# Performance work log

Measured on AMD Instinct MI355X. Metric: run time of the kernel, lower is better.

The kernel has to match this reference:

```python
import jax, jax.numpy as jnp
import numpy as np

S, B, V, E, H, T = 256, 32, 50000, 300, 256, 32  # seq, batch, vocab, emb, lstm hidden, num_tags


def _lstm_dir(x, w_ih, w_hh, b_ih, b_hh, reverse):
    # x: [S, B, in]; gates in PyTorch order i, f, g, o
    Bm, Hm = x.shape[1], w_hh.shape[1]
    def step(carry, xt):
        h, c = carry
        g = xt @ w_ih.T + b_ih + h @ w_hh.T + b_hh  # [B, 4H]
        i, f, gg, o = jnp.split(g, 4, axis=-1)
        c = jax.nn.sigmoid(f) * c + jax.nn.sigmoid(i) * jnp.tanh(gg)
        h = jax.nn.sigmoid(o) * jnp.tanh(c)
        return (h, c), h
    init = (jnp.zeros((Bm, Hm), x.dtype), jnp.zeros((Bm, Hm), x.dtype))
    _, hs = jax.lax.scan(step, init, x, reverse=reverse)
    return hs  # [S, B, H]


def _crf_loss(em, tags, start, trans, end):
    # em: [S, B, T]; torchcrf log-likelihood, reduction='sum', full mask
    bidx = jnp.arange(em.shape[1])
    # numerator (gold path score)
    emit = jnp.take_along_axis(em, tags[:, :, None], axis=2)[..., 0].sum(0)  # [B]
    tr = trans[tags[:-1], tags[1:]].sum(0)  # [B]
    num = start[tags[0]] + emit + tr + end[tags[-1]]
    # denominator (forward algorithm)
    def step(alpha, e):
        alpha = jax.nn.logsumexp(alpha[:, :, None] + trans[None] + e[:, None, :], axis=1)
        return alpha, None
    alpha0 = start[None] + em[0]  # [B, T]
    alpha, _ = jax.lax.scan(step, alpha0, em[1:])
    logZ = jax.nn.logsumexp(alpha + end[None], axis=-1)  # [B]
    return -(num - logZ).sum()


def _viterbi(em, start, trans, end):
    def step(s, e):
        cand = s[:, :, None] + trans[None]           # [B, T_prev, T_cur]
        return cand.max(1) + e, cand.argmax(1)        # score [B,T], backptr [B,T]
    score0 = start[None] + em[0]
    score, hist = jax.lax.scan(step, score0, em[1:])  # hist: [S-1, B, T]
    last = jnp.argmax(score + end[None], axis=-1)     # [B]
    def back(tag, bp):
        prev = jnp.take_along_axis(bp, tag[:, None], axis=1)[:, 0]
        return prev, prev
    _, path_head = jax.lax.scan(back, last, hist, reverse=True)  # [S-1, B]
    return jnp.concatenate([path_head, last[None]], axis=0).astype(jnp.int32)  # [S, B]


def setup_inputs():
    key = jax.random.key(0)
    ks = jax.random.split(key, 32)
    def n(k, shape, s=0.1):
        return (jax.random.normal(k, shape, jnp.float32) * s)
    inp = {
        'words': jax.random.randint(ks[0], (S, B), 0, V),
        'chars': jax.random.randint(ks[1], (S, B, 16), 0, 100),
        'tags': jax.random.randint(ks[2], (S, B), 0, T),
        'emb_table': n(ks[3], (V, E)),
        'fc_w': n(ks[4], (T, 2 * H), float(np.sqrt(2.0 / (T + 2 * H)))),
        'fc_b': n(ks[5], (T,), float(np.sqrt(1.0 / T))),
        'crf_start': n(ks[6], (T,)),
        'crf_end': n(ks[7], (T,)),
        'crf_trans': n(ks[8], (T, T)),
    }
    i = 9
    for l, din in ((0, E), (1, 2 * H)):
        for d in ('f', 'b'):
            inp[f'w_ih_l{l}{d}'] = n(ks[i], (4 * H, din)); i += 1
            inp[f'w_hh_l{l}{d}'] = n(ks[i], (4 * H, H)); i += 1
            inp[f'b_ih_l{l}{d}'] = n(ks[i], (4 * H,)); i += 1
            inp[f'b_hh_l{l}{d}'] = n(ks[i], (4 * H,)); i += 1
    return inp


def reference(words, chars, tags, emb_table, fc_w, fc_b, crf_start, crf_end, crf_trans,
              w_ih_l0f, w_hh_l0f, b_ih_l0f, b_hh_l0f,
              w_ih_l0b, w_hh_l0b, b_ih_l0b, b_hh_l0b,
              w_ih_l1f, w_hh_l1f, b_ih_l1f, b_hh_l1f,
              w_ih_l1b, w_hh_l1b, b_ih_l1b, b_hh_l1b):
    # chars / char CNN are unused in the original forward()
    x = emb_table[words]                                   # [S, B, E]
    h0 = jnp.concatenate([
        _lstm_dir(x, w_ih_l0f, w_hh_l0f, b_ih_l0f, b_hh_l0f, False),
        _lstm_dir(x, w_ih_l0b, w_hh_l0b, b_ih_l0b, b_hh_l0b, True)], axis=-1)
    h1 = jnp.concatenate([
        _lstm_dir(h0, w_ih_l1f, w_hh_l1f, b_ih_l1f, b_hh_l1f, False),
        _lstm_dir(h0, w_ih_l1b, w_hh_l1b, b_ih_l1b, b_hh_l1b, True)], axis=-1)  # [S, B, 2H]
    em = h1 @ fc_w.T + fc_b                                # emissions [S, B, T]
    crf_out = _viterbi(em, crf_start, crf_trans, crf_end)  # [S, B] int32
    crf_loss = _crf_loss(em, tags, crf_start, crf_trans, crf_end)
    return crf_out, crf_loss
```

## Files before the change

### kernel.cpp

```cpp
#include <hip/hip_runtime.h>
#include <stdint.h>

#define S_ 256
#define B_ 32
#define H_ 256
#define G4_ 1024
#define HXW (16*132)

typedef short bf16x8 __attribute__((ext_vector_type(8)));
typedef float f32x4  __attribute__((ext_vector_type(4)));

__device__ __forceinline__ unsigned f2bf(float f){
  unsigned u = __float_as_uint(f);
  return (u + 0x7fffu + ((u >> 16) & 1u)) >> 16;
}
__device__ __forceinline__ float bfl(unsigned u){ return __uint_as_float(u << 16); }
__device__ __forceinline__ float bfh(unsigned u){ return __uint_as_float(u & 0xffff0000u); }
__device__ __forceinline__ float sigf(float x){ return 1.0f / (1.0f + __expf(-x)); }
__device__ __forceinline__ float thf(float x){
  x = fminf(fmaxf(x, -15.0f), 15.0f);
  float e = __expf(2.0f * x);
  return (e - 1.0f) / (e + 1.0f);
}

__device__ __forceinline__ int hval_ok(unsigned long long v){
  return (((unsigned)v & (unsigned)(v >> 32)) & 0x40004000u) == 0x40004000u;
}

__global__ __launch_bounds__(320) void k_prep(const int* __restrict__ words,
                                              const float* __restrict__ emb,
                                              unsigned short* __restrict__ x,
                                              unsigned* __restrict__ hbuf0){
  int row = blockIdx.x;
  int e = threadIdx.x;
  int w = words[row];
  x[row * 320 + e] = (e < 300) ? (unsigned short)f2bf(emb[w * 300 + e]) : 0;
  if (e < 256) hbuf0[row * 256 + e] = 0;
}

__global__ __launch_bounds__(256) void k_packw(
    const float* __restrict__ w0f, const float* __restrict__ w0b,
    const float* __restrict__ w1f, const float* __restrict__ w1b,
    const float* __restrict__ fw,
    unsigned short* __restrict__ wb0f, unsigned short* __restrict__ wb0b,
    unsigned short* __restrict__ wb1f, unsigned short* __restrict__ wb1b,
    unsigned short* __restrict__ fcwb){
  int r = blockIdx.x, tid = threadIdx.x;
  if (r < 2048){
    int rr = r & 1023;
    const float* src = (r < 1024) ? w0f : w0b;
    unsigned short* dst = (r < 1024) ? wb0f : wb0b;
    for (int e = tid; e < 320; e += 256)
      dst[rr * 320 + e] = (e < 300) ? (unsigned short)f2bf(src[rr * 300 + e]) : 0;
  } else if (r < 4096){
    int rr = r & 1023;
    const float* src = (r < 3072) ? w1f : w1b;
    unsigned short* dst = (r < 3072) ? wb1f : wb1b;
    for (int e = tid; e < 512; e += 256)
      dst[rr * 512 + e] = (unsigned short)f2bf(src[rr * 512 + e]);
  } else {
    int rr = r - 4096;
    for (int e = tid; e < 512; e += 256)
      fcwb[rr * 512 + e] = (unsigned short)f2bf(fw[rr * 512 + e]);
  }
}

__global__ __launch_bounds__(256) void k_gemm_bf2(
    const unsigned short* __restrict__ A, int lda, int nSteps,
    const unsigned short* __restrict__ Bf, const unsigned short* __restrict__ Bb,
    const float* __restrict__ b1f, const float* __restrict__ b2f,
    const float* __restrict__ b1b, const float* __restrict__ b2b,
    float* __restrict__ Cf, float* __restrict__ Cb){
  const int z = blockIdx.z;
  const unsigned short* __restrict__ B = z ? Bb : Bf;
  const float* __restrict__ bias1 = z ? b1b : b1f;
  const float* __restrict__ bias2 = z ? b2b : b2f;
  float* __restrict__ C = z ? Cb : Cf;

  __shared__ __align__(16) unsigned As[64 * 20];
  __shared__ __align__(16) unsigned Bs[128 * 20];
  const int tid = threadIdx.x;
  const int w = tid >> 6, lane = tid & 63;
  const int quad = lane >> 4, coln = lane & 15;
  const int m0 = blockIdx.y * 64, n0 = blockIdx.x * 128;

  f32x4 acc[8];
  #pragma unroll
  for (int i = 0; i < 8; ++i){ acc[i][0]=0.f; acc[i][1]=0.f; acc[i][2]=0.f; acc[i][3]=0.f; }

  for (int kt = 0; kt < nSteps; ++kt){
    int k0 = kt * 32;
    __syncthreads();
    {
      int row = tid >> 2, part = tid & 3;
      *(uint4*)&As[row * 20 + part * 4] =
          *(const uint4*)(A + (size_t)(m0 + row) * lda + k0 + part * 8);
    }
    #pragma unroll
    for (int i = 0; i < 2; ++i){
      int idx = tid + 256 * i;
      int row = idx >> 2, part = idx & 3;
      *(uint4*)&Bs[row * 20 + part * 4] =
          *(const uint4*)(B + (size_t)(n0 + row) * lda + k0 + part * 8);
    }
    __syncthreads();
    union { uint4 q; bf16x8 v; } au;
    au.q = *(const uint4*)&As[(w * 16 + coln) * 20 + quad * 4];
    #pragma unroll
    for (int nt = 0; nt < 8; ++nt){
      union { uint4 q; bf16x8 v; } bu;
      bu.q = *(const uint4*)&Bs[(nt * 16 + coln) * 20 + quad * 4];
      acc[nt] = __builtin_amdgcn_mfma_f32_16x16x32_bf16(au.v, bu.v, acc[nt], 0, 0, 0);
    }
  }
  #pragma unroll
  for (int nt = 0; nt < 8; ++nt){
    int col = n0 + nt * 16 + coln;
    float bs = bias1[col] + bias2[col];
    #pragma unroll
    for (int reg = 0; reg < 4; ++reg)
      C[(size_t)(m0 + w * 16 + quad * 4 + reg) * 1024 + col] = acc[nt][reg] + bs;
  }
}

__global__ __launch_bounds__(256, 1) void k_lstm2(
    const float* __restrict__ Gf, const float* __restrict__ Gb,
    const float* __restrict__ Whf, const float* __restrict__ Whb,
    unsigned* __restrict__ hbuf,
    unsigned short* __restrict__ Hout)
{
  __shared__ __align__(16) unsigned hx[2 * HXW];
  const int wg  = blockIdx.x;
  const int dir = wg >> 3, n = (wg >> 1) & 3, bh = wg & 1;
  const float* __restrict__ G  = dir ? Gb : Gf;
  const float* __restrict__ Wh = dir ? Whb : Whf;
  const int tid  = threadIdx.x;
  const int w    = tid >> 6;
  const int lane = tid & 63;
  const int quad = lane >> 4, coln = lane & 15;

  bf16x8 Wr[32];
  #pragma unroll
  for (int ks = 0; ks < 8; ++ks){
    #pragma unroll
    for (int gt = 0; gt < 4; ++gt){
      const float* wp = Wh + (size_t)(gt * 256 + (n << 6) + (w << 4) + coln) * 256
                        + ks * 32 + quad * 8;
      float4 a = *(const float4*)wp;
      float4 b = *(const float4*)(wp + 4);
      union { unsigned u[4]; bf16x8 v; } tu;
      tu.u[0] = f2bf(a.x) | (f2bf(a.y) << 16);
      tu.u[1] = f2bf(a.z) | (f2bf(a.w) << 16);
      tu.u[2] = f2bf(b.x) | (f2bf(b.y) << 16);
      tu.u[3] = f2bf(b.z) | (f2bf(b.w) << 16);
      Wr[ks * 4 + gt] = tu.v;
    }
  }

  const int gu  = (n << 6) + (w << 4) + coln;
  const int mrw = quad << 2;

  float c0 = 0.f, c1 = 0.f, c2 = 0.f, c3 = 0.f;

  for (int t = 0; t < 256; ++t){
    int s = dir ? (255 - t) : t;
    f32x4 acc[4];
    #pragma unroll
    for (int gt = 0; gt < 4; ++gt){
      const float* gp = G + (size_t)(s * 32 + bh * 16 + mrw) * 1024 + gt * 256 + gu;
      f32x4 a;
      a[0] = gp[0]; a[1] = gp[1024]; a[2] = gp[2048]; a[3] = gp[3072];
      acc[gt] = a;
    }
    unsigned* hxr = &hx[(t & 1) * HXW];
    if (t > 0){
      const unsigned* hb = hbuf + (((size_t)(t - 1) * 2 + dir) * 2 + bh) * 2048;
      int row = tid >> 4, kk = tid & 15;
      int n1 = (n + 1) & 3, n2 = (n + 2) & 3, n3 = (n + 3) & 3;
      const unsigned long long* p1 =
          (const unsigned long long*)(hb + row * 128 + n1 * 32 + kk * 2);
      const unsigned long long* p2 =
          (const unsigned long long*)(hb + row * 128 + n2 * 32 + kk * 2);
      const unsigned long long* p3 =
          (const unsigned long long*)(hb + row * 128 + n3 * 32 + kk * 2);
      unsigned long long v1, v2, v3;
      do {
        v1 = __hip_atomic_load(p1, __ATOMIC_RELAXED, __HIP_MEMORY_SCOPE_AGENT);
        v2 = __hip_atomic_load(p2, __ATOMIC_RELAXED, __HIP_MEMORY_SCOPE_AGENT);
        v3 = __hip_atomic_load(p3, __ATOMIC_RELAXED, __HIP_MEMORY_SCOPE_AGENT);
      } while (!(hval_ok(v1) && hval_ok(v2) && hval_ok(v3)));
      hxr[row * 132 + n1 * 32 + kk * 2]     = (unsigned)v1 & 0xBFFFBFFFu;
      hxr[row * 132 + n1 * 32 + kk * 2 + 1] = (unsigned)(v1 >> 32) & 0xBFFFBFFFu;
      hxr[row * 132 + n2 * 32 + kk * 2]     = (unsigned)v2 & 0xBFFFBFFFu;
      hxr[row * 132 + n2 * 32 + kk * 2 + 1] = (unsigned)(v2 >> 32) & 0xBFFFBFFFu;
      hxr[row * 132 + n3 * 32 + kk * 2]     = (unsigned)v3 & 0xBFFFBFFFu;
      hxr[row * 132 + n3 * 32 + kk * 2 + 1] = (unsigned)(v3 >> 32) & 0xBFFFBFFFu;
      __syncthreads();
      #pragma unroll
      for (int ks = 0; ks < 8; ++ks){
        union { uint4 q; bf16x8 v; } tu;
        tu.q = *(const uint4*)&hxr[coln * 132 + ks * 16 + quad * 4];
        #pragma unroll
        for (int gt = 0; gt < 4; ++gt)
          acc[gt] = __builtin_amdgcn_mfma_f32_16x16x32_bf16(tu.v, Wr[ks * 4 + gt],
                                                            acc[gt], 0, 0, 0);
      }
    }
    unsigned* hxw = &hx[((t + 1) & 1) * HXW];
    unsigned* hw  = hbuf + (((size_t)t * 2 + dir) * 2 + bh) * 2048;
    float cc[4] = {c0, c1, c2, c3};
    #pragma unroll
    for (int reg = 0; reg < 4; ++reg){
      float gi = sigf(acc[0][reg]);
      float gf = sigf(acc[1][reg]);
      float gg = thf (acc[2][reg]);
      float go = sigf(acc[3][reg]);
      float cv = gf * cc[reg] + gi * gg;
      cc[reg] = cv;
      float hv = go * thf(cv);
      unsigned hb16 = f2bf(hv);
      unsigned other = (unsigned)__shfl_xor((int)hb16, 1);
      if (!(coln & 1)){
        unsigned pair = hb16 | (other << 16);
        hxw[(mrw + reg) * 132 + (gu >> 1)] = pair;
        if (t < 255)
          __hip_atomic_store(hw + (mrw + reg) * 128 + (gu >> 1),
                             pair | 0x40004000u,
                             __ATOMIC_RELAXED, __HIP_MEMORY_SCOPE_AGENT);
      }
      Hout[(size_t)(s * 32 + bh * 16 + mrw + reg) * 512 + dir * 256 + gu] =
          (unsigned short)hb16;
    }
    c0 = cc[0]; c1 = cc[1]; c2 = cc[2]; c3 = cc[3];
  }
}

__global__ __launch_bounds__(64) void k_fc(const unsigned short* __restrict__ h1,
                                           const unsigned short* __restrict__ fw,
                                           const float* __restrict__ fb,
                                           float* __restrict__ em){
  int row = blockIdx.x;
  int lane = threadIdx.x;
  int tag = lane & 31, half = lane >> 5;
  const uint4* hp = (const uint4*)(h1 + (size_t)row * 512 + half * 256);
  const uint4* wp = (const uint4*)(fw + (size_t)tag * 512 + half * 256);
  float acc = 0.0f;
  #pragma unroll 8
  for (int i = 0; i < 32; ++i){
    uint4 h = hp[i], v = wp[i];
    acc += bfl(h.x) * bfl(v.x) + bfh(h.x) * bfh(v.x)
         + bfl(h.y) * bfl(v.y) + bfh(h.y) * bfh(v.y)
         + bfl(h.z) * bfl(v.z) + bfh(h.z) * bfh(v.z)
         + bfl(h.w) * bfl(v.w) + bfh(h.w) * bfh(v.w);
  }
  acc += __shfl_down(acc, 32);
  if (half == 0) em[row * 32 + tag] = acc + fb[tag];
}

__global__ __launch_bounds__(64) void k_crf(const float* __restrict__ em,
                                            const int* __restrict__ tags,
                                            const float* __restrict__ start,
                                            const float* __restrict__ trans,
                                            const float* __restrict__ endv,
                                            int* __restrict__ path,
                                            float* __restrict__ lossb){
  __shared__ float tr[1024];
  __shared__ float sc[32], sc2[32];
  __shared__ unsigned char bp[255][32];
  int b = blockIdx.x & 31, mode = blockIdx.x >> 5;
  int t = threadIdx.x;
  for (int i = t; i < 1024; i += 64) tr[i] = trans[i];
  if (t < 32) sc[t] = start[t] + em[b * 32 + t];
  __syncthreads();
  if (mode == 0){
    for (int s = 1; s < 256; ++s){
      if (t < 32){
        float best = -1e30f; int bi = 0;
        for (int p = 0; p < 32; ++p){
          float v = sc[p] + tr[p * 32 + t];
          if (v > best){ best = v; bi = p; }
        }
        sc2[t] = best + em[(s * 32 + b) * 32 + t];
        bp[s - 1][t] = (unsigned char)bi;
      }
      __syncthreads();
      if (t < 32) sc[t] = sc2[t];
      __syncthreads();
    }
    if (t == 0){
      float best = -1e30f; int bi = 0;
      for (int p = 0; p < 32; ++p){
        float v = sc[p] + endv[p];
        if (v > best){ best = v; bi = p; }
      }
      int cur = bi;
      path[255 * 32 + b] = cur;
      for (int s = 254; s >= 0; --s){
        cur = bp[s][cur];
        path[s * 32 + b] = cur;
      }
    }
  } else {
    for (int s = 1; s < 256; ++s){
      if (t < 32){
        float m = -1e30f;
        for (int p = 0; p < 32; ++p){ float v = sc[p] + tr[p * 32 + t]; m = fmaxf(m, v); }
        float ss = 0.0f;
        for (int p = 0; p < 32; ++p){ ss += __expf(sc[p] + tr[p * 32 + t] - m); }
        sc2[t] = m + __logf(ss) + em[(s * 32 + b) * 32 + t];
      }
      __syncthreads();
      if (t < 32) sc[t] = sc2[t];
      __syncthreads();
    }
    float nsum = 0.0f;
    for (int s = t; s < 256; s += 64){
      int tg = tags[s * 32 + b];
      nsum += em[(s * 32 + b) * 32 + tg];
      if (s == 0) nsum += start[tg];
      else        nsum += tr[tags[(s - 1) * 32 + b] * 32 + tg];
      if (s == 255) nsum += endv[tg];
    }
    #pragma unroll
    for (int off = 32; off >= 1; off >>= 1) nsum += __shfl_down(nsum, off);
    if (t == 0){
      float m = -1e30f;
      for (int p = 0; p < 32; ++p) m = fmaxf(m, sc[p] + endv[p]);
      float ss = 0.0f;
      for (int p = 0; p < 32; ++p) ss += __expf(sc[p] + endv[p] - m);
      lossb[b] = m + __logf(ss) - nsum;
    }
  }
}

__global__ __launch_bounds__(64) void k_final(const float* __restrict__ lossb,
                                              float* __restrict__ outp){
  float v = (threadIdx.x < 32) ? lossb[threadIdx.x] : 0.0f;
  #pragma unroll
  for (int off = 32; off >= 1; off >>= 1) v += __shfl_down(v, off);
  if (threadIdx.x == 0) outp[0] = v;
}

extern "C" void kernel_launch(void* const* d_in, const int* in_sizes, int n_in,
                              void* d_out, int out_size, void* d_ws, size_t ws_size,
                              hipStream_t stream){
  const int*   words  = (const int*)d_in[0];
  const int*   tags   = (const int*)d_in[2];
  const float* emb    = (const float*)d_in[3];
  const float* fcw    = (const float*)d_in[4];
  const float* fcb    = (const float*)d_in[5];
  const float* cstart = (const float*)d_in[6];
  const float* cend   = (const float*)d_in[7];
  const float* ctrans = (const float*)d_in[8];
  const float* w_ih[4] = {(const float*)d_in[9],  (const float*)d_in[13],
                          (const float*)d_in[17], (const float*)d_in[21]};
  const float* w_hh[4] = {(const float*)d_in[10], (const float*)d_in[14],
                          (const float*)d_in[18], (const float*)d_in[22]};
  const float* b_ih[4] = {(const float*)d_in[11], (const float*)d_in[15],
                          (const float*)d_in[19], (const float*)d_in[23]};
  const float* b_hh[4] = {(const float*)d_in[12], (const float*)d_in[16],
                          (const float*)d_in[20], (const float*)d_in[24]};

  char* base = (char*)d_ws;
  unsigned short* x    = (unsigned short*)base;
  float* Gf            = (float*)(base + 5242880);
  float* Gb            = (float*)(base + 38797312);
  unsigned short* h0   = (unsigned short*)(base + 72351744);
  unsigned short* h1   = (unsigned short*)(base + 80740352);
  unsigned short* wb0f = (unsigned short*)(base + 89128960);
  unsigned short* wb0b = (unsigned short*)(base + 89784320);
  unsigned short* wb1f = (unsigned short*)(base + 90439680);
  unsigned short* wb1b = (unsigned short*)(base + 91488256);
  unsigned short* fcwb = (unsigned short*)(base + 92536832);
  float* lossb         = (float*)(base + 92569600);
  float* em            = Gf;
  unsigned* hbuf0 = (unsigned*)h1;
  unsigned* hbuf1 = (unsigned*)h0;

  k_prep<<<8192, 320, 0, stream>>>(words, emb, x, hbuf0);
  k_packw<<<4128, 256, 0, stream>>>(w_ih[0], w_ih[1], w_ih[2], w_ih[3], fcw,
                                    wb0f, wb0b, wb1f, wb1b, fcwb);

  k_gemm_bf2<<<dim3(8, 128, 2), 256, 0, stream>>>(x, 320, 10, wb0f, wb0b,
                                                  b_ih[0], b_hh[0], b_ih[1], b_hh[1],
                                                  Gf, Gb);
  k_lstm2<<<16, 256, 0, stream>>>(Gf, Gb, w_hh[0], w_hh[1], hbuf0, h0);

  k_gemm_bf2<<<dim3(8, 128, 2), 256, 0, stream>>>(h0, 512, 16, wb1f, wb1b,
                                                  b_ih[2], b_hh[2], b_ih[3], b_hh[3],
                                                  Gf, Gb);
  k_lstm2<<<16, 256, 0, stream>>>(Gf, Gb, w_hh[2], w_hh[3], hbuf1, h1);

  k_fc<<<8192, 64, 0, stream>>>(h1, fcwb, fcb, em);

  k_crf<<<64, 64, 0, stream>>>(em, tags, cstart, ctrans, cend, (int*)d_out, lossb);
  k_final<<<1, 64, 0, stream>>>(lossb, ((float*)d_out) + (out_size - 1));
}
```

Baseline: 1.498 ms.

## Overlap gate loads with h exchange in LSTM and use MFMA for FC

In the recurrent LSTM kernel, the per-step input-gate loads from G and the previous step's Hout store now happen after the spin-wait on the neighbours' hidden state. This keeps that memory traffic off the critical path before the barrier, and the hbuf atomic stores are issued before the LDS writes. The gate pre-activations are added after the MFMA accumulation rather than used as its initial value. Separately, the FC emission projection is rewritten as a 16x16x32 bf16 MFMA tile kernel with the FC weights staged in LDS, using 128 blocks instead of 8192 tiny ones.

```diff
diff --git a/kernel.cpp b/kernel.cpp
--- a/kernel.cpp
+++ b/kernel.cpp
@@ -161,18 +161,15 @@
   const int mrw = quad << 2;
 
   float c0 = 0.f, c1 = 0.f, c2 = 0.f, c3 = 0.f;
+  unsigned prevH[4];
+  int prevS = -1;
 
   for (int t = 0; t < 256; ++t){
     int s = dir ? (255 - t) : t;
+    unsigned* hxr = &hx[(t & 1) * HXW];
+    float gv[4][4];
     f32x4 acc[4];
-    #pragma unroll
-    for (int gt = 0; gt < 4; ++gt){
-      const float* gp = G + (size_t)(s * 32 + bh * 16 + mrw) * 1024 + gt * 256 + gu;
-      f32x4 a;
-      a[0] = gp[0]; a[1] = gp[1024]; a[2] = gp[2048]; a[3] = gp[3072];
-      acc[gt] = a;
-    }
-    unsigned* hxr = &hx[(t & 1) * HXW];
+
     if (t > 0){
       const unsigned* hb = hbuf + (((size_t)(t - 1) * 2 + dir) * 2 + bh) * 2048;
       int row = tid >> 4, kk = tid & 15;
@@ -189,6 +186,19 @@
         v2 = __hip_atomic_load(p2, __ATOMIC_RELAXED, __HIP_MEMORY_SCOPE_AGENT);
         v3 = __hip_atomic_load(p3, __ATOMIC_RELAXED, __HIP_MEMORY_SCOPE_AGENT);
       } while (!(hval_ok(v1) && hval_ok(v2) && hval_ok(v3)));
+      __builtin_amdgcn_sched_barrier(0);
+
+      #pragma unroll
+      for (int gt = 0; gt < 4; ++gt){
+        const float* gp = G + (size_t)(s * 32 + bh * 16 + mrw) * 1024 + gt * 256 + gu;
+        gv[gt][0] = gp[0]; gv[gt][1] = gp[1024];
+        gv[gt][2] = gp[2048]; gv[gt][3] = gp[3072];
+      }
+      #pragma unroll
+      for (int reg = 0; reg < 4; ++reg)
+        Hout[(size_t)(prevS * 32 + bh * 16 + mrw + reg) * 512 + dir * 256 + gu] =
+            (unsigned short)prevH[reg];
+
       hxr[row * 132 + n1 * 32 + kk * 2]     = (unsigned)v1 & 0xBFFFBFFFu;
       hxr[row * 132 + n1 * 32 + kk * 2 + 1] = (unsigned)(v1 >> 32) & 0xBFFFBFFFu;
       hxr[row * 132 + n2 * 32 + kk * 2]     = (unsigned)v2 & 0xBFFFBFFFu;
@@ -197,6 +207,10 @@
       hxr[row * 132 + n3 * 32 + kk * 2 + 1] = (unsigned)(v3 >> 32) & 0xBFFFBFFFu;
       __syncthreads();
       #pragma unroll
+      for (int gt = 0; gt < 4; ++gt){
+        acc[gt][0] = 0.f; acc[gt][1] = 0.f; acc[gt][2] = 0.f; acc[gt][3] = 0.f;
+      }
+      #pragma unroll
       for (int ks = 0; ks < 8; ++ks){
         union { uint4 q; bf16x8 v; } tu;
         tu.q = *(const uint4*)&hxr[coln * 132 + ks * 16 + quad * 4];
@@ -205,56 +219,98 @@
           acc[gt] = __builtin_amdgcn_mfma_f32_16x16x32_bf16(tu.v, Wr[ks * 4 + gt],
                                                             acc[gt], 0, 0, 0);
       }
-    }
+    } else {
+      #pragma unroll
+      for (int gt = 0; gt < 4; ++gt){
+        const float* gp = G + (size_t)(s * 32 + bh * 16 + mrw) * 1024 + gt * 256 + gu;
+        gv[gt][0] = gp[0]; gv[gt][1] = gp[1024];
+        gv[gt][2] = gp[2048]; gv[gt][3] = gp[3072];
+      }
+      #pragma unroll
+      for (int gt = 0; gt < 4; ++gt){
+        acc[gt][0] = 0.f; acc[gt][1] = 0.f; acc[gt][2] = 0.f; acc[gt][3] = 0.f;
+      }
+    }
+
     unsigned* hxw = &hx[((t + 1) & 1) * HXW];
     unsigned* hw  = hbuf + (((size_t)t * 2 + dir) * 2 + bh) * 2048;
     float cc[4] = {c0, c1, c2, c3};
+    unsigned hbv[4], pr[4];
     #pragma unroll
     for (int reg = 0; reg < 4; ++reg){
-      float gi = sigf(acc[0][reg]);
-      float gf = sigf(acc[1][reg]);
-      float gg = thf (acc[2][reg]);
-      float go = sigf(acc[3][reg]);
+      float gi = sigf(acc[0][reg] + gv[0][reg]);
+      float gf = sigf(acc[1][reg] + gv[1][reg]);
+      float gg = thf (acc[2][reg] + gv[2][reg]);
+      float go = sigf(acc[3][reg] + gv[3][reg]);
       float cv = gf * cc[reg] + gi * gg;
       cc[reg] = cv;
       float hv = go * thf(cv);
-      unsigned hb16 = f2bf(hv);
-      unsigned other = (unsigned)__shfl_xor((int)hb16, 1);
-      if (!(coln & 1)){
-        unsigned pair = hb16 | (other << 16);
-        hxw[(mrw + reg) * 132 + (gu >> 1)] = pair;
-        if (t < 255)
+      hbv[reg] = f2bf(hv);
+      unsigned other = (unsigned)__shfl_xor((int)hbv[reg], 1);
+      pr[reg] = hbv[reg] | (other << 16);
+    }
+    if (!(coln & 1)){
+      if (t < 255){
+        #pragma unroll
+        for (int reg = 0; reg < 4; ++reg)
           __hip_atomic_store(hw + (mrw + reg) * 128 + (gu >> 1),
-                             pair | 0x40004000u,
+                             pr[reg] | 0x40004000u,
                              __ATOMIC_RELAXED, __HIP_MEMORY_SCOPE_AGENT);
       }
-      Hout[(size_t)(s * 32 + bh * 16 + mrw + reg) * 512 + dir * 256 + gu] =
-          (unsigned short)hb16;
-    }
+      #pragma unroll
+      for (int reg = 0; reg < 4; ++reg)
+        hxw[(mrw + reg) * 132 + (gu >> 1)] = pr[reg];
+    }
+    #pragma unroll
+    for (int reg = 0; reg < 4; ++reg) prevH[reg] = hbv[reg];
+    prevS = s;
     c0 = cc[0]; c1 = cc[1]; c2 = cc[2]; c3 = cc[3];
   }
-}
-
-__global__ __launch_bounds__(64) void k_fc(const unsigned short* __restrict__ h1,
-                                           const unsigned short* __restrict__ fw,
-                                           const float* __restrict__ fb,
-                                           float* __restrict__ em){
-  int row = blockIdx.x;
-  int lane = threadIdx.x;
-  int tag = lane & 31, half = lane >> 5;
-  const uint4* hp = (const uint4*)(h1 + (size_t)row * 512 + half * 256);
-  const uint4* wp = (const uint4*)(fw + (size_t)tag * 512 + half * 256);
-  float acc = 0.0f;
-  #pragma unroll 8
-  for (int i = 0; i < 32; ++i){
-    uint4 h = hp[i], v = wp[i];
-    acc += bfl(h.x) * bfl(v.x) + bfh(h.x) * bfh(v.x)
-         + bfl(h.y) * bfl(v.y) + bfh(h.y) * bfh(v.y)
-         + bfl(h.z) * bfl(v.z) + bfh(h.z) * bfh(v.z)
-         + bfl(h.w) * bfl(v.w) + bfh(h.w) * bfh(v.w);
-  }
-  acc += __shfl_down(acc, 32);
-  if (half == 0) em[row * 32 + tag] = acc + fb[tag];
+  #pragma unroll
+  for (int reg = 0; reg < 4; ++reg)
+    Hout[(size_t)(prevS * 32 + bh * 16 + mrw + reg) * 512 + dir * 256 + gu] =
+        (unsigned short)prevH[reg];
+}
+
+__global__ __launch_bounds__(256) void k_fc(const unsigned short* __restrict__ h1,
+                                            const unsigned short* __restrict__ fw,
+                                            const float* __restrict__ fb,
+                                            float* __restrict__ em){
+  __shared__ __align__(16) unsigned Bs[32 * 260];
+  const int tid = threadIdx.x;
+  const int w = tid >> 6, lane = tid & 63;
+  const int quad = lane >> 4, coln = lane & 15;
+  const int m0 = blockIdx.x * 64;
+
+  for (int i = tid; i < 2048; i += 256){
+    int r = i >> 6, part = i & 63;
+    *(uint4*)&Bs[r * 260 + part * 4] = *(const uint4*)(fw + r * 512 + part * 8);
+  }
+  __syncthreads();
+
+  f32x4 acc[2];
+  acc[0][0]=0.f; acc[0][1]=0.f; acc[0][2]=0.f; acc[0][3]=0.f;
+  acc[1][0]=0.f; acc[1][1]=0.f; acc[1][2]=0.f; acc[1][3]=0.f;
+  const unsigned short* arow = h1 + (size_t)(m0 + w * 16 + coln) * 512;
+  #pragma unroll
+  for (int ks = 0; ks < 16; ++ks){
+    union { uint4 q; bf16x8 v; } au;
+    au.q = *(const uint4*)(arow + ks * 32 + quad * 8);
+    #pragma unroll
+    for (int nt = 0; nt < 2; ++nt){
+      union { uint4 q; bf16x8 v; } bu;
+      bu.q = *(const uint4*)&Bs[(nt * 16 + coln) * 260 + ks * 16 + quad * 4];
+      acc[nt] = __builtin_amdgcn_mfma_f32_16x16x32_bf16(au.v, bu.v, acc[nt], 0, 0, 0);
+    }
+  }
+  #pragma unroll
+  for (int nt = 0; nt < 2; ++nt){
+    int col = nt * 16 + coln;
+    float bias = fb[col];
+    #pragma unroll
+    for (int reg = 0; reg < 4; ++reg)
+      em[(size_t)(m0 + w * 16 + quad * 4 + reg) * 32 + col] = acc[nt][reg] + bias;
+  }
 }
 
 __global__ __launch_bounds__(64) void k_crf(const float* __restrict__ em,
@@ -391,7 +447,7 @@
                                                   Gf, Gb);
   k_lstm2<<<16, 256, 0, stream>>>(Gf, Gb, w_hh[2], w_hh[3], hbuf1, h1);
 
-  k_fc<<<8192, 64, 0, stream>>>(h1, fcwb, fcb, em);
+  k_fc<<<128, 256, 0, stream>>>(h1, fcwb, fcb, em);
 
   k_crf<<<64, 64, 0, stream>>>(em, tags, cstart, ctrans, cend, (int*)d_out, lossb);
   k_final<<<1, 64, 0, stream>>>(lossb, ((float*)d_out) + (out_size - 1));
```

Measured after the change: 1.487 ms. Within noise of the previous version (-0.7%).
